# Performance work log

Hardware: AMD Instinct MI355X
Metric: run time of the kernel (lower is better)

Reference implementation:

```python
import jax, jax.numpy as jnp
import numpy as np

B, S, D, H = 2, 2048, 1024, 16
HEAD_DIM = D // H
WINDOW = 256
DILATION = 1
NEG = jnp.float32(-1e9)


def _build_attn_mask(seq_len):
    # Faithful port of torch _build_attn_mask for causal=True, stencil kind='local'.
    idx = jnp.arange(seq_len)
    diff = idx[None, :] - idx[:, None]  # diff[i, j] = j - i (torch diff is idx.unsqueeze(0)-idx.unsqueeze(1))
    # causal: -inf strictly above diagonal (j > i)
    mask = jnp.where(diff > 0, -jnp.inf, 0.0).astype(jnp.float32)
    # stencil allow: |diff| <= window and |diff| % dilation == 0
    cond = (jnp.abs(diff) <= WINDOW) & (jnp.abs(diff) % DILATION == 0)
    allowed = jnp.where(cond, 0.0, -jnp.inf).astype(jnp.float32)
    # torch.maximum: allow() can UNMASK causally-masked positions inside the window
    mask = jnp.maximum(mask, allowed)
    # clamp(min=-1e9)
    return jnp.maximum(mask, NEG)


def setup_inputs() -> dict:
    key = jax.random.key(0)
    k = jax.random.split(key, 5)
    return {
        "x": jax.random.normal(k[0], (B, S, D), dtype=jnp.float32),
        "in_proj_w": jax.random.normal(k[1], (3 * D, D), dtype=jnp.float32) * (D ** -0.5),
        "in_proj_b": jax.random.normal(k[2], (3 * D,), dtype=jnp.float32) * 0.02,
        "out_proj_w": jax.random.normal(k[3], (D, D), dtype=jnp.float32) * (D ** -0.5),
        "out_proj_b": jax.random.normal(k[4], (D,), dtype=jnp.float32) * 0.02,
    }


def reference(x, in_proj_w, in_proj_b, out_proj_w, out_proj_b):
    b, s, d = x.shape
    # fused qkv projection (torch nn.MultiheadAttention in_proj)
    qkv = x @ in_proj_w.T + in_proj_b  # [b, s, 3d]
    q, k, v = jnp.split(qkv, 3, axis=-1)

    def to_heads(t):
        return t.reshape(b, s, H, HEAD_DIM).transpose(0, 2, 1, 3)  # [b, h, s, hd]

    q, k, v = to_heads(q), to_heads(k), to_heads(v)
    scale = jnp.float32(HEAD_DIM) ** -0.5
    scores = jnp.einsum("bhqd,bhkd->bhqk", q * scale, k)  # [b, h, s, s]
    mask = _build_attn_mask(s)  # [s, s]
    scores = scores + mask[None, None, :, :]
    attn = jax.nn.softmax(scores, axis=-1)
    out = jnp.einsum("bhqk,bhkd->bhqd", attn, v)  # [b, h, s, hd]
    out = out.transpose(0, 2, 1, 3).reshape(b, s, d)
    return out @ out_proj_w.T + out_proj_b
```

## Files before the change

### kernel.cpp

```cpp
#include <hip/hip_runtime.h>
#include <cstddef>

#define BATCH   2
#define SEQ     2048
#define DMODEL  1024
#define NH      16
#define HDIM    64
#define WIN     256
#define MTOT    4096

typedef __bf16 bf16;
typedef __attribute__((ext_vector_type(8)))  __bf16 bf16x8;
typedef __attribute__((ext_vector_type(4)))  float  f32x4;
typedef __attribute__((ext_vector_type(16))) float  f32x16;

#define GLOAD_LDS(gp, lp) __builtin_amdgcn_global_load_lds( \
    (const __attribute__((address_space(1))) void*)(gp),    \
    (__attribute__((address_space(3))) void*)(lp), 16, 0, 0)

__device__ __forceinline__ float fast_exp2(float x) {
#if __has_builtin(__builtin_amdgcn_exp2f)
  return __builtin_amdgcn_exp2f(x);
#else
  float r; asm("v_exp_f32 %0, %1" : "=v"(r) : "v"(x)); return r;
#endif
}

__device__ __forceinline__ unsigned int cvtpk_bf16(float lo, float hi) {
  unsigned int r;
  asm("v_cvt_pk_bf16_f32 %0, %1, %2" : "=v"(r) : "v"(lo), "v"(hi));
  return r;
}

__global__ __launch_bounds__(256)
void cvt_all(const float* __restrict__ x, const float* __restrict__ w1,
             const float* __restrict__ w2, bf16* __restrict__ xh,
             bf16* __restrict__ xl, bf16* __restrict__ w1h,
             bf16* __restrict__ w1l, bf16* __restrict__ w2h,
             bf16* __restrict__ w2l) {
  const int bid = blockIdx.x;
  const float* s; bf16 *hp, *lp; int base;
  if (bid < 2048)      { s = x;  hp = xh;  lp = xl;  base = bid * 2048; }
  else if (bid < 3584) { s = w1; hp = w1h; lp = w1l; base = (bid - 2048) * 2048; }
  else                 { s = w2; hp = w2h; lp = w2l; base = (bid - 3584) * 2048; }
  const int i = base + threadIdx.x * 8;
  float4 a = *(const float4*)(s + i);
  float4 c = *(const float4*)(s + i + 4);
  const float f[8] = {a.x, a.y, a.z, a.w, c.x, c.y, c.z, c.w};
  bf16x8 vh, vl;
#pragma unroll
  for (int j = 0; j < 8; ++j) {
    bf16 hh = (bf16)f[j];
    vh[j] = hh;
    vl[j] = (bf16)(f[j] - (float)hh);
  }
  *(bf16x8*)(hp + i) = vh;
  *(bf16x8*)(lp + i) = vl;
}

__global__ __launch_bounds__(256, 4)
void gemm_qkv_fused(const bf16* __restrict__ xh, const bf16* __restrict__ xl,
                    const bf16* __restrict__ w1h, const bf16* __restrict__ w1l,
                    const float* __restrict__ b1,
                    bf16* __restrict__ Qh, bf16* __restrict__ Ql,
                    bf16* __restrict__ Kt, bf16* __restrict__ Vt) {
  __shared__ bf16 sAh[128 * 32];
  __shared__ bf16 sAl[128 * 32];
  __shared__ bf16 sBh[128 * 32];
  __shared__ bf16 sBl[64 * 32];

  const int t = threadIdx.x, w = t >> 6, lane = t & 63;
  const int ln15 = lane & 15, quad = lane >> 4;
  const int drow = lane >> 2;
  const int dkswz = (((lane & 3) ^ ((drow >> 1) & 3)) * 8);
  const int qswz = ((quad ^ ((ln15 >> 1) & 3)) * 8);
  const int bid = blockIdx.x;

  if (bid < 512) {
    const int g = bid & 7, s = bid >> 3;
    const int bm = (g * 4 + (s >> 4)) * 128;
    const int bn = (s & 15) * 64;

    f32x4 acc[2][4];
#pragma unroll
    for (int i = 0; i < 2; ++i)
#pragma unroll
      for (int j = 0; j < 4; ++j)
#pragma unroll
        for (int r = 0; r < 4; ++r) acc[i][j][r] = 0.f;

    for (int k0 = 0; k0 < DMODEL; k0 += 32) {
      __syncthreads();
#pragma unroll
      for (int half = 0; half < 2; ++half) {
        const int r = w * 32 + half * 16 + drow;
        const size_t goffA = (size_t)(bm + r) * DMODEL + k0 + dkswz;
        const int loff = (w * 32 + half * 16) * 32;
        GLOAD_LDS(xh + goffA, sAh + loff);
        GLOAD_LDS(xl + goffA, sAl + loff);
      }
      {
        const int r = w * 16 + drow;
        const size_t goffB = (size_t)(bn + r) * DMODEL + k0 + dkswz;
        const int loff = (w * 16) * 32;
        GLOAD_LDS(w1h + goffB, sBh + loff);
        GLOAD_LDS(w1l + goffB, sBl + loff);
      }
      __syncthreads();

      bf16x8 afh[2], afl[2], bfh[4], bfl[4];
#pragma unroll
      for (int mt = 0; mt < 2; ++mt) {
        const int off = (w * 32 + mt * 16 + ln15) * 32 + qswz;
        afh[mt] = *(const bf16x8*)&sAh[off];
        afl[mt] = *(const bf16x8*)&sAl[off];
      }
#pragma unroll
      for (int nt = 0; nt < 4; ++nt) {
        const int off = (nt * 16 + ln15) * 32 + qswz;
        bfh[nt] = *(const bf16x8*)&sBh[off];
        bfl[nt] = *(const bf16x8*)&sBl[off];
      }
#pragma unroll
      for (int mt = 0; mt < 2; ++mt)
#pragma unroll
        for (int nt = 0; nt < 4; ++nt) {
          acc[mt][nt] = __builtin_amdgcn_mfma_f32_16x16x32_bf16(afh[mt], bfh[nt], acc[mt][nt], 0, 0, 0);
          acc[mt][nt] = __builtin_amdgcn_mfma_f32_16x16x32_bf16(afh[mt], bfl[nt], acc[mt][nt], 0, 0, 0);
          acc[mt][nt] = __builtin_amdgcn_mfma_f32_16x16x32_bf16(afl[mt], bfh[nt], acc[mt][nt], 0, 0, 0);
        }
    }

    float bbcol[4];
#pragma unroll
    for (int nt = 0; nt < 4; ++nt) bbcol[nt] = b1[bn + nt * 16 + ln15];

#pragma unroll
    for (int mt = 0; mt < 2; ++mt)
#pragma unroll
      for (int r = 0; r < 4; ++r) {
        const size_t grow = (size_t)(bm + w * 32 + mt * 16 + quad * 4 + r);
#pragma unroll
        for (int nt = 0; nt < 4; ++nt) {
          const int col = bn + nt * 16 + ln15;
          const float v = acc[mt][nt][r] + bbcol[nt];
          const bf16 hh = (bf16)v;
          Qh[grow * 1024 + col] = hh;
          Ql[grow * 1024 + col] = (bf16)(v - (float)hh);
        }
      }
  } else if (bid < 768) {
    const int kid = bid - 512;
    const int g = kid & 7, s = kid >> 3;
    const int bm = (g * 4 + (s >> 3)) * 128;
    const int bn = 1024 + (s & 7) * 128;
    const int wrow = (w & 1) * 64, wcol = (w >> 1) * 64;

    f32x4 acc[4][4];
#pragma unroll
    for (int i = 0; i < 4; ++i)
#pragma unroll
      for (int j = 0; j < 4; ++j)
#pragma unroll
        for (int r = 0; r < 4; ++r) acc[i][j][r] = 0.f;

    for (int k0 = 0; k0 < DMODEL; k0 += 32) {
      __syncthreads();
#pragma unroll
      for (int half = 0; half < 2; ++half) {
        const int r = w * 32 + half * 16 + drow;
        const int loff = (w * 32 + half * 16) * 32;
        GLOAD_LDS(xh + (size_t)(bm + r) * DMODEL + k0 + dkswz, sAh + loff);
        GLOAD_LDS(w1h + (size_t)(bn + r) * DMODEL + k0 + dkswz, sBh + loff);
      }
      __syncthreads();

      bf16x8 af[4], bf[4];
#pragma unroll
      for (int mt = 0; mt < 4; ++mt)
        af[mt] = *(const bf16x8*)&sAh[(wrow + mt * 16 + ln15) * 32 + qswz];
#pragma unroll
      for (int nt = 0; nt < 4; ++nt)
        bf[nt] = *(const bf16x8*)&sBh[(wcol + nt * 16 + ln15) * 32 + qswz];
#pragma unroll
      for (int mt = 0; mt < 4; ++mt)
#pragma unroll
        for (int nt = 0; nt < 4; ++nt)
          acc[mt][nt] = __builtin_amdgcn_mfma_f32_16x16x32_bf16(af[mt], bf[nt], acc[mt][nt], 0, 0, 0);
    }

    float bbcol[4];
#pragma unroll
    for (int nt = 0; nt < 4; ++nt) bbcol[nt] = b1[bn + wcol + nt * 16 + ln15];

#pragma unroll
    for (int mt = 0; mt < 4; ++mt)
#pragma unroll
      for (int r = 0; r < 4; ++r) {
        const size_t grow = (size_t)(bm + wrow + mt * 16 + quad * 4 + r);
        const int btok = (int)(grow >> 11), key = (int)(grow & 2047);
        const int kt = key >> 6, kw = key & 63;
#pragma unroll
        for (int nt = 0; nt < 4; ++nt) {
          const int col = bn + wcol + nt * 16 + ln15;
          const float v = acc[mt][nt][r] + bbcol[nt];
          const int hh2 = (col - 1024) >> 6, d = col & 63;
          const size_t addr = ((size_t)((btok * 16 + hh2) * 32 + kt) << 12)
                            + (((kw >> 5) * 4 + (d >> 4)) << 9)
                            + ((((d >> 3) & 1) << 5) + (kw & 31)) * 8 + (d & 7);
          Kt[addr] = (bf16)v;
        }
      }
  } else {
    const int vid = bid - 768;
    const int bm = (vid >> 5) * 128, bn = (vid & 31) * 128;
    const int wrow = (w & 1) * 64, wcol = (w >> 1) * 64;
    const bf16* Ah = w1h + 2048 * 1024;
    const float* bias = b1 + 2048;

    f32x4 acc[4][4];
#pragma unroll
    for (int i = 0; i < 4; ++i)
#pragma unroll
      for (int j = 0; j < 4; ++j)
#pragma unroll
        for (int r = 0; r < 4; ++r) acc[i][j][r] = 0.f;

    for (int k0 = 0; k0 < DMODEL; k0 += 32) {
      __syncthreads();
#pragma unroll
      for (int half = 0; half < 2; ++half) {
        const int r = w * 32 + half * 16 + drow;
        const int loff = (w * 32 + half * 16) * 32;
        GLOAD_LDS(Ah + (size_t)(bm + r) * DMODEL + k0 + dkswz, sAh + loff);
        GLOAD_LDS(xh + (size_t)(bn + r) * DMODEL + k0 + dkswz, sBh + loff);
      }
      __syncthreads();

      bf16x8 af[4], bf[4];
#pragma unroll
      for (int mt = 0; mt < 4; ++mt)
        af[mt] = *(const bf16x8*)&sAh[(wrow + mt * 16 + ln15) * 32 + qswz];
#pragma unroll
      for (int nt = 0; nt < 4; ++nt)
        bf[nt] = *(const bf16x8*)&sBh[(wcol + nt * 16 + ln15) * 32 + qswz];
#pragma unroll
      for (int mt = 0; mt < 4; ++mt)
#pragma unroll
        for (int nt = 0; nt < 4; ++nt)
          acc[mt][nt] = __builtin_amdgcn_mfma_f32_16x16x32_bf16(af[mt], bf[nt], acc[mt][nt], 0, 0, 0);
    }

#pragma unroll
    for (int mt = 0; mt < 4; ++mt)
#pragma unroll
      for (int r = 0; r < 4; ++r) {
        const size_t grow = (size_t)(bm + wrow + mt * 16 + quad * 4 + r);
        const float brow = bias[grow];
        const int hh2 = (int)(grow >> 6), d = (int)(grow & 63);
#pragma unroll
        for (int nt = 0; nt < 4; ++nt) {
          const int col = bn + wcol + nt * 16 + ln15;
          const float v = acc[mt][nt][r] + brow;
          const int btok = col >> 11, key = col & 2047;
          const int kt = key >> 6, kw = key & 63;
          const size_t addr = ((size_t)((btok * 16 + hh2) * 32 + kt) << 12)
                            + (((d >> 5) * 4 + (kw >> 4)) << 9)
                            + ((((kw >> 3) & 1) << 5) + (d & 31)) * 8 + (kw & 7);
          Vt[addr] = (bf16)v;
        }
      }
  }
}

__global__ __launch_bounds__(256)
void gemm_out64(const bf16* __restrict__ Ah, const bf16* __restrict__ Al,
                const bf16* __restrict__ Bh, const bf16* __restrict__ Bl,
                const float* __restrict__ bias, float* __restrict__ Cf) {
  __shared__ bf16 sAh[64 * 64];
  __shared__ bf16 sAl[64 * 64];
  __shared__ bf16 sBh[64 * 64];
  __shared__ bf16 sBl[64 * 64];

  const int t = threadIdx.x, w = t >> 6, lane = t & 63;
  const int ln15 = lane & 15, quad = lane >> 4;
  const int bid = blockIdx.x;
  const int g = bid & 7, s = bid >> 3;
  const int bm = (g * 8 + (s >> 4)) * 64;
  const int bn = (s & 15) * 64;
  const int wrow = (w & 1) * 32, wcol = (w >> 1) * 32;
  const int drow8 = lane >> 3;
  const int dcol8 = (((lane & 7) ^ drow8) * 8);

  f32x4 acc[2][2];
#pragma unroll
  for (int i = 0; i < 2; ++i)
#pragma unroll
    for (int j = 0; j < 2; ++j)
#pragma unroll
      for (int r = 0; r < 4; ++r) acc[i][j][r] = 0.f;

  for (int k0 = 0; k0 < DMODEL; k0 += 64) {
    __syncthreads();
#pragma unroll
    for (int p = 0; p < 2; ++p) {
      const int r = w * 16 + p * 8 + drow8;
      const size_t goffA = (size_t)(bm + r) * DMODEL + k0 + dcol8;
      const size_t goffB = (size_t)(bn + r) * DMODEL + k0 + dcol8;
      const int loff = (w * 16 + p * 8) * 64;
      GLOAD_LDS(Ah + goffA, sAh + loff);
      GLOAD_LDS(Al + goffA, sAl + loff);
      GLOAD_LDS(Bh + goffB, sBh + loff);
      GLOAD_LDS(Bl + goffB, sBl + loff);
    }
    __syncthreads();

#pragma unroll
    for (int ks = 0; ks < 2; ++ks) {
      bf16x8 afh[2], afl[2], bfh[2], bfl[2];
#pragma unroll
      for (int mt = 0; mt < 2; ++mt) {
        const int row = wrow + mt * 16 + ln15;
        const int off = row * 64 + (((ks * 4 + quad) ^ (row & 7)) * 8);
        afh[mt] = *(const bf16x8*)&sAh[off];
        afl[mt] = *(const bf16x8*)&sAl[off];
      }
#pragma unroll
      for (int nt = 0; nt < 2; ++nt) {
        const int row = wcol + nt * 16 + ln15;
        const int off = row * 64 + (((ks * 4 + quad) ^ (row & 7)) * 8);
        bfh[nt] = *(const bf16x8*)&sBh[off];
        bfl[nt] = *(const bf16x8*)&sBl[off];
      }
#pragma unroll
      for (int mt = 0; mt < 2; ++mt)
#pragma unroll
        for (int nt = 0; nt < 2; ++nt) {
          acc[mt][nt] = __builtin_amdgcn_mfma_f32_16x16x32_bf16(afh[mt], bfh[nt], acc[mt][nt], 0, 0, 0);
          acc[mt][nt] = __builtin_amdgcn_mfma_f32_16x16x32_bf16(afh[mt], bfl[nt], acc[mt][nt], 0, 0, 0);
          acc[mt][nt] = __builtin_amdgcn_mfma_f32_16x16x32_bf16(afl[mt], bfh[nt], acc[mt][nt], 0, 0, 0);
        }
    }
  }

  float bbcol[2];
#pragma unroll
  for (int nt = 0; nt < 2; ++nt) bbcol[nt] = bias[bn + wcol + nt * 16 + ln15];

#pragma unroll
  for (int mt = 0; mt < 2; ++mt)
#pragma unroll
    for (int r = 0; r < 4; ++r) {
      const size_t grow = (size_t)(bm + wrow + mt * 16 + quad * 4 + r);
#pragma unroll
      for (int nt = 0; nt < 2; ++nt) {
        const int col = bn + wcol + nt * 16 + ln15;
        Cf[grow * 1024 + col] = acc[mt][nt][r] + bbcol[nt];
      }
    }
}

__global__ __launch_bounds__(64, 2)
void attn_mfma(const bf16* __restrict__ Qh, const bf16* __restrict__ Ql,
               const bf16* __restrict__ Kt, const bf16* __restrict__ Vt,
               bf16* __restrict__ Omh, bf16* __restrict__ Oml) {
  const int lane = threadIdx.x & 63;
  const int ln31 = lane & 31, half = lane >> 5;
  const int bid = blockIdx.x;
  const int j = bid & 31;
  const int bh = ((j & 7) << 2) | (j >> 3);
  const int c  = 63 - (bid >> 5);
  const int b = bh >> 4, h = bh & 15;
  const int i0w = c * 32;
  const int lim = i0w + WIN;

  bf16x8 qh[4], ql[4];
  {
    const size_t rowQ = (size_t)(b * SEQ + i0w + ln31);
#pragma unroll
    for (int ks = 0; ks < 4; ++ks) {
      bf16x8 vh = *(const bf16x8*)(Qh + rowQ * 1024 + h * 64 + ks * 16 + half * 8);
      bf16x8 vl = *(const bf16x8*)(Ql + rowQ * 1024 + h * 64 + ks * 16 + half * 8);
#pragma unroll
      for (int jj = 0; jj < 8; ++jj) {
        float f = ((float)vh[jj] + (float)vl[jj]) * 0.1803368801111204f;
        bf16 hh = (bf16)f;
        qh[ks][jj] = hh;
        ql[ks][jj] = (bf16)(f - (float)hh);
      }
    }
  }

  f32x16 accO0, accO1;
#pragma unroll
  for (int r = 0; r < 16; ++r) { accO0[r] = 0.f; accO1[r] = 0.f; }
  float lsum = 0.f;

  const bf16* KtBH = Kt + ((size_t)(b * 16 + h) << 17);
  const bf16* VtBH = Vt + ((size_t)(b * 16 + h) << 17);
  const int lane8 = lane * 8;

  const int nkt = min((i0w + 31 + WIN) / 64 + 1, SEQ / 64);

  for (int kt = 0; kt < nkt; ++kt) {
    const bf16* Kb = KtBH + ((size_t)kt << 12);
    const bf16* Vb = VtBH + ((size_t)kt << 12);

    bf16x8 kf[8], vf[8];
#pragma unroll
    for (int s = 0; s < 8; ++s) {
      kf[s] = *(const bf16x8*)&Kb[(s << 9) + lane8];
      vf[s] = *(const bf16x8*)&Vb[(s << 9) + lane8];
    }

    f32x16 S0, S1;
#pragma unroll
    for (int r = 0; r < 16; ++r) { S0[r] = 0.f; S1[r] = 0.f; }
    __builtin_amdgcn_s_setprio(1);
#pragma unroll
    for (int ks = 0; ks < 4; ++ks) {
      S0 = __builtin_amdgcn_mfma_f32_32x32x16_bf16(kf[ks], qh[ks], S0, 0, 0, 0);
      S0 = __builtin_amdgcn_mfma_f32_32x32x16_bf16(kf[ks], ql[ks], S0, 0, 0, 0);
      S1 = __builtin_amdgcn_mfma_f32_32x32x16_bf16(kf[4 + ks], qh[ks], S1, 0, 0, 0);
      S1 = __builtin_amdgcn_mfma_f32_32x32x16_bf16(kf[4 + ks], ql[ks], S1, 0, 0, 0);
    }
    __builtin_amdgcn_s_setprio(0);

    const int j0 = kt * 64;
    bf16x8 pa[4];
#pragma unroll
    for (int cc = 0; cc < 2; ++cc) {
      f32x16& S = cc ? S1 : S0;
      const int base = j0 + cc * 32 - lim;
      const bool may = (base + 31 > 0);
#pragma unroll
      for (int r = 0; r < 16; ++r) {
        const int kr = (r & 3) + 8 * (r >> 2) + 4 * half;
        float pv = fast_exp2(S[r]);
        if (may && (kr + base > ln31)) pv = 0.f;
        S[r] = pv;
        lsum += pv;
      }
      unsigned int W0[4], W1[4];
#pragma unroll
      for (int g = 0; g < 4; ++g) {
        W0[g] = cvtpk_bf16(S[4 * g + 0], S[4 * g + 1]);
        W1[g] = cvtpk_bf16(S[4 * g + 2], S[4 * g + 3]);
      }
#pragma unroll
      for (int f = 0; f < 2; ++f) {
        auto s0 = __builtin_amdgcn_permlane32_swap(W0[2 * f], W0[2 * f + 1], false, false);
        auto s1 = __builtin_amdgcn_permlane32_swap(W1[2 * f], W1[2 * f + 1], false, false);
        union { unsigned int w[4]; bf16x8 v; } u;
        u.w[0] = (unsigned int)s0[0];
        u.w[1] = (unsigned int)s1[0];
        u.w[2] = (unsigned int)s0[1];
        u.w[3] = (unsigned int)s1[1];
        pa[cc * 2 + f] = u.v;
      }
    }

    __builtin_amdgcn_s_setprio(1);
#pragma unroll
    for (int ks = 0; ks < 4; ++ks) {
      accO0 = __builtin_amdgcn_mfma_f32_32x32x16_bf16(pa[ks], vf[ks], accO0, 0, 0, 0);
      accO1 = __builtin_amdgcn_mfma_f32_32x32x16_bf16(pa[ks], vf[4 + ks], accO1, 0, 0, 0);
    }
    __builtin_amdgcn_s_setprio(0);
  }

  lsum += __shfl_xor(lsum, 32, 64);
#pragma unroll
  for (int r = 0; r < 16; ++r) {
    const int rl = (r & 3) + 8 * (r >> 2) + 4 * half;
    const float lv = __shfl(lsum, rl, 64);
    const float inv = 1.0f / lv;
    const size_t grow = (size_t)(b * SEQ + i0w + rl);
    const int col0 = h * 64 + ln31;
    const float v0 = accO0[r] * inv;
    const float v1 = accO1[r] * inv;
    const bf16 h0 = (bf16)v0, h1 = (bf16)v1;
    Omh[grow * DMODEL + col0]      = h0;
    Oml[grow * DMODEL + col0]      = (bf16)(v0 - (float)h0);
    Omh[grow * DMODEL + col0 + 32] = h1;
    Oml[grow * DMODEL + col0 + 32] = (bf16)(v1 - (float)h1);
  }
}

extern "C" void kernel_launch(void* const* d_in, const int* in_sizes, int n_in,
                              void* d_out, int out_size, void* d_ws, size_t ws_size,
                              hipStream_t stream) {
  const float* x  = (const float*)d_in[0];
  const float* w1 = (const float*)d_in[1];
  const float* b1 = (const float*)d_in[2];
  const float* w2 = (const float*)d_in[3];
  const float* b2 = (const float*)d_in[4];
  float* out = (float*)d_out;

  char* ws = (char*)d_ws;
  bf16* Qh   = (bf16*)(ws + 0);
  bf16* Ql   = (bf16*)(ws + 8388608);
  bf16* Kt   = (bf16*)(ws + 16777216);
  bf16* Vt   = (bf16*)(ws + 25165824);
  bf16* xh   = (bf16*)(ws + 33554432);
  bf16* xl   = (bf16*)(ws + 41943040);
  bf16* w1h  = (bf16*)(ws + 50331648);
  bf16* w1l  = (bf16*)(ws + 56623104);
  bf16* w2h  = (bf16*)(ws + 62914560);
  bf16* w2l  = (bf16*)(ws + 65011712);
  bf16* Omh  = xh;
  bf16* Oml  = xl;

  cvt_all<<<dim3(4096), 256, 0, stream>>>(x, w1, w2, xh, xl, w1h, w1l, w2h, w2l);

  gemm_qkv_fused<<<dim3(1024), 256, 0, stream>>>(
      xh, xl, w1h, w1l, b1, Qh, Ql, Kt, Vt);

  attn_mfma<<<dim3(2048), 64, 0, stream>>>(Qh, Ql, Kt, Vt, Omh, Oml);

  gemm_out64<<<dim3(1024), 256, 0, stream>>>(
      Omh, Oml, w2h, w2l, b2, out);
}
```

Before: 221.9 us.

## Double-buffer LDS tiles in QKV GEMM to overlap loads with MFMA

Converts the three QKV GEMM paths (Q split-precision, K, V) to double-buffered shared-memory staging. The next k-slice is prefetched with global_load_lds into the alternate buffer while MFMAs run on the current one, and one barrier per iteration replaces two. Shared memory doubles and the launch-bounds occupancy hint drops from 4 to 2 blocks per CU, which costs latency hiding across waves. Correctness depends on the single barrier also waiting for the async LDS loads to finish, which is not guaranteed without an explicit vmcnt wait.

After: 223.5 us. No clear change (+0.7%).

```diff
diff --git a/kernel.cpp b/kernel.cpp
--- a/kernel.cpp
+++ b/kernel.cpp
@@ -58,16 +58,16 @@
   *(bf16x8*)(lp + i) = vl;
 }
 
-__global__ __launch_bounds__(256, 4)
+__global__ __launch_bounds__(256, 2)
 void gemm_qkv_fused(const bf16* __restrict__ xh, const bf16* __restrict__ xl,
                     const bf16* __restrict__ w1h, const bf16* __restrict__ w1l,
                     const float* __restrict__ b1,
                     bf16* __restrict__ Qh, bf16* __restrict__ Ql,
                     bf16* __restrict__ Kt, bf16* __restrict__ Vt) {
-  __shared__ bf16 sAh[128 * 32];
-  __shared__ bf16 sAl[128 * 32];
-  __shared__ bf16 sBh[128 * 32];
-  __shared__ bf16 sBl[64 * 32];
+  __shared__ bf16 sAh[2][128 * 32];
+  __shared__ bf16 sAl[2][128 * 32];
+  __shared__ bf16 sBh[2][128 * 32];
+  __shared__ bf16 sBl[2][64 * 32];
 
   const int t = threadIdx.x, w = t >> 6, lane = t & 63;
   const int ln15 = lane & 15, quad = lane >> 4;
@@ -89,37 +89,56 @@
 #pragma unroll
         for (int r = 0; r < 4; ++r) acc[i][j][r] = 0.f;
 
+#pragma unroll
+    for (int half = 0; half < 2; ++half) {
+      const int r = w * 32 + half * 16 + drow;
+      const size_t goffA = (size_t)(bm + r) * DMODEL + dkswz;
+      const int loff = (w * 32 + half * 16) * 32;
+      GLOAD_LDS(xh + goffA, &sAh[0][loff]);
+      GLOAD_LDS(xl + goffA, &sAl[0][loff]);
+    }
+    {
+      const int r = w * 16 + drow;
+      const size_t goffB = (size_t)(bn + r) * DMODEL + dkswz;
+      const int loff = (w * 16) * 32;
+      GLOAD_LDS(w1h + goffB, &sBh[0][loff]);
+      GLOAD_LDS(w1l + goffB, &sBl[0][loff]);
+    }
+    __syncthreads();
+
     for (int k0 = 0; k0 < DMODEL; k0 += 32) {
-      __syncthreads();
-#pragma unroll
-      for (int half = 0; half < 2; ++half) {
-        const int r = w * 32 + half * 16 + drow;
-        const size_t goffA = (size_t)(bm + r) * DMODEL + k0 + dkswz;
-        const int loff = (w * 32 + half * 16) * 32;
-        GLOAD_LDS(xh + goffA, sAh + loff);
-        GLOAD_LDS(xl + goffA, sAl + loff);
-      }
-      {
-        const int r = w * 16 + drow;
-        const size_t goffB = (size_t)(bn + r) * DMODEL + k0 + dkswz;
-        const int loff = (w * 16) * 32;
-        GLOAD_LDS(w1h + goffB, sBh + loff);
-        GLOAD_LDS(w1l + goffB, sBl + loff);
-      }
-      __syncthreads();
+      const int cur = (k0 >> 5) & 1;
+      if (k0 + 32 < DMODEL) {
+        const int nxt = cur ^ 1;
+#pragma unroll
+        for (int half = 0; half < 2; ++half) {
+          const int r = w * 32 + half * 16 + drow;
+          const size_t goffA = (size_t)(bm + r) * DMODEL + (k0 + 32) + dkswz;
+          const int loff = (w * 32 + half * 16) * 32;
+          GLOAD_LDS(xh + goffA, &sAh[nxt][loff]);
+          GLOAD_LDS(xl + goffA, &sAl[nxt][loff]);
+        }
+        {
+          const int r = w * 16 + drow;
+          const size_t goffB = (size_t)(bn + r) * DMODEL + (k0 + 32) + dkswz;
+          const int loff = (w * 16) * 32;
+          GLOAD_LDS(w1h + goffB, &sBh[nxt][loff]);
+          GLOAD_LDS(w1l + goffB, &sBl[nxt][loff]);
+        }
+      }
 
       bf16x8 afh[2], afl[2], bfh[4], bfl[4];
 #pragma unroll
       for (int mt = 0; mt < 2; ++mt) {
         const int off = (w * 32 + mt * 16 + ln15) * 32 + qswz;
-        afh[mt] = *(const bf16x8*)&sAh[off];
-        afl[mt] = *(const bf16x8*)&sAl[off];
+        afh[mt] = *(const bf16x8*)&sAh[cur][off];
+        afl[mt] = *(const bf16x8*)&sAl[cur][off];
       }
 #pragma unroll
       for (int nt = 0; nt < 4; ++nt) {
         const int off = (nt * 16 + ln15) * 32 + qswz;
-        bfh[nt] = *(const bf16x8*)&sBh[off];
-        bfl[nt] = *(const bf16x8*)&sBl[off];
+        bfh[nt] = *(const bf16x8*)&sBh[cur][off];
+        bfl[nt] = *(const bf16x8*)&sBl[cur][off];
       }
 #pragma unroll
       for (int mt = 0; mt < 2; ++mt)
@@ -129,6 +148,7 @@
           acc[mt][nt] = __builtin_amdgcn_mfma_f32_16x16x32_bf16(afh[mt], bfl[nt], acc[mt][nt], 0, 0, 0);
           acc[mt][nt] = __builtin_amdgcn_mfma_f32_16x16x32_bf16(afl[mt], bfh[nt], acc[mt][nt], 0, 0, 0);
         }
+      __syncthreads();
     }
 
     float bbcol[4];
@@ -164,29 +184,41 @@
 #pragma unroll
         for (int r = 0; r < 4; ++r) acc[i][j][r] = 0.f;
 
+#pragma unroll
+    for (int half = 0; half < 2; ++half) {
+      const int r = w * 32 + half * 16 + drow;
+      const int loff = (w * 32 + half * 16) * 32;
+      GLOAD_LDS(xh + (size_t)(bm + r) * DMODEL + dkswz, &sAh[0][loff]);
+      GLOAD_LDS(w1h + (size_t)(bn + r) * DMODEL + dkswz, &sBh[0][loff]);
+    }
+    __syncthreads();
+
     for (int k0 = 0; k0 < DMODEL; k0 += 32) {
-      __syncthreads();
-#pragma unroll
-      for (int half = 0; half < 2; ++half) {
-        const int r = w * 32 + half * 16 + drow;
-        const int loff = (w * 32 + half * 16) * 32;
-        GLOAD_LDS(xh + (size_t)(bm + r) * DMODEL + k0 + dkswz, sAh + loff);
-        GLOAD_LDS(w1h + (size_t)(bn + r) * DMODEL + k0 + dkswz, sBh + loff);
-      }
-      __syncthreads();
+      const int cur = (k0 >> 5) & 1;
+      if (k0 + 32 < DMODEL) {
+        const int nxt = cur ^ 1;
+#pragma unroll
+        for (int half = 0; half < 2; ++half) {
+          const int r = w * 32 + half * 16 + drow;
+          const int loff = (w * 32 + half * 16) * 32;
+          GLOAD_LDS(xh + (size_t)(bm + r) * DMODEL + (k0 + 32) + dkswz, &sAh[nxt][loff]);
+          GLOAD_LDS(w1h + (size_t)(bn + r) * DMODEL + (k0 + 32) + dkswz, &sBh[nxt][loff]);
+        }
+      }
 
       bf16x8 af[4], bf[4];
 #pragma unroll
       for (int mt = 0; mt < 4; ++mt)
-        af[mt] = *(const bf16x8*)&sAh[(wrow + mt * 16 + ln15) * 32 + qswz];
+        af[mt] = *(const bf16x8*)&sAh[cur][(wrow + mt * 16 + ln15) * 32 + qswz];
 #pragma unroll
       for (int nt = 0; nt < 4; ++nt)
-        bf[nt] = *(const bf16x8*)&sBh[(wcol + nt * 16 + ln15) * 32 + qswz];
+        bf[nt] = *(const bf16x8*)&sBh[cur][(wcol + nt * 16 + ln15) * 32 + qswz];
 #pragma unroll
       for (int mt = 0; mt < 4; ++mt)
 #pragma unroll
         for (int nt = 0; nt < 4; ++nt)
           acc[mt][nt] = __builtin_amdgcn_mfma_f32_16x16x32_bf16(af[mt], bf[nt], acc[mt][nt], 0, 0, 0);
+      __syncthreads();
     }
 
     float bbcol[4];
@@ -226,29 +258,41 @@
 #pragma unroll
         for (int r = 0; r < 4; ++r) acc[i][j][r] = 0.f;
 
+#pragma unroll
+    for (int half = 0; half < 2; ++half) {
+      const int r = w * 32 + half * 16 + drow;
+      const int loff = (w * 32 + half * 16) * 32;
+      GLOAD_LDS(Ah + (size_t)(bm + r) * DMODEL + dkswz, &sAh[0][loff]);
+      GLOAD_LDS(xh + (size_t)(bn + r) * DMODEL + dkswz, &sBh[0][loff]);
+    }
+    __syncthreads();
+
     for (int k0 = 0; k0 < DMODEL; k0 += 32) {
-      __syncthreads();
-#pragma unroll
-      for (int half = 0; half < 2; ++half) {
-        const int r = w * 32 + half * 16 + drow;
-        const int loff = (w * 32 + half * 16) * 32;
-        GLOAD_LDS(Ah + (size_t)(bm + r) * DMODEL + k0 + dkswz, sAh + loff);
-        GLOAD_LDS(xh + (size_t)(bn + r) * DMODEL + k0 + dkswz, sBh + loff);
-      }
-      __syncthreads();
+      const int cur = (k0 >> 5) & 1;
+      if (k0 + 32 < DMODEL) {
+        const int nxt = cur ^ 1;
+#pragma unroll
+        for (int half = 0; half < 2; ++half) {
+          const int r = w * 32 + half * 16 + drow;
+          const int loff = (w * 32 + half * 16) * 32;
+          GLOAD_LDS(Ah + (size_t)(bm + r) * DMODEL + (k0 + 32) + dkswz, &sAh[nxt][loff]);
+          GLOAD_LDS(xh + (size_t)(bn + r) * DMODEL + (k0 + 32) + dkswz, &sBh[nxt][loff]);
+        }
+      }
 
       bf16x8 af[4], bf[4];
 #pragma unroll
       for (int mt = 0; mt < 4; ++mt)
-        af[mt] = *(const bf16x8*)&sAh[(wrow + mt * 16 + ln15) * 32 + qswz];
+        af[mt] = *(const bf16x8*)&sAh[cur][(wrow + mt * 16 + ln15) * 32 + qswz];
 #pragma unroll
       for (int nt = 0; nt < 4; ++nt)
-        bf[nt] = *(const bf16x8*)&sBh[(wcol + nt * 16 + ln15) * 32 + qswz];
+        bf[nt] = *(const bf16x8*)&sBh[cur][(wcol + nt * 16 + ln15) * 32 + qswz];
 #pragma unroll
       for (int mt = 0; mt < 4; ++mt)
 #pragma unroll
         for (int nt = 0; nt < 4; ++nt)
           acc[mt][nt] = __builtin_amdgcn_mfma_f32_16x16x32_bf16(af[mt], bf[nt], acc[mt][nt], 0, 0, 0);
+      __syncthreads();
     }
 
 #pragma unroll
```
